# Optimization experiments

Hardware: AMD Instinct MI355X
Metric: run time of the kernel (lower is better)

The kernel has to match this reference:

```python
import jax, jax.numpy as jnp
import numpy as np

B, T, D = 32, 256, 256  # batch, input_length, output_dim (input_dim == output_dim)
SCALE = 0.06  # ~ 1/sqrt(D) glorot-ish init so LSTM gates don't saturate


def hard_sigmoid(x):
    # Keras-1 default inner_activation for LSTM
    return jnp.clip(0.2 * x + 0.5, 0.0, 1.0)


def lstm_cell(x_t, h, c, W, U, b, d):
    # Keras gate order: i, f, c(g), o
    z = x_t @ W + h @ U + b
    i = hard_sigmoid(z[:, :d])
    f = hard_sigmoid(z[:, d:2 * d])
    g = jnp.tanh(z[:, 2 * d:3 * d])
    o = hard_sigmoid(z[:, 3 * d:])
    c_new = f * c + i * g
    h_new = o * jnp.tanh(c_new)
    return h_new, c_new


def setup_inputs() -> dict:
    key = jax.random.key(0)
    ks = jax.random.split(key, 7)
    x = jax.random.normal(ks[0], (B, T, D), dtype=jnp.float32)
    reader_W = jax.random.normal(ks[1], (D, 4 * D), dtype=jnp.float32) * SCALE
    reader_U = jax.random.normal(ks[2], (D, 4 * D), dtype=jnp.float32) * SCALE
    reader_b = jnp.zeros((4 * D,), jnp.float32)
    writer_W = jax.random.normal(ks[3], (2 * D, 4 * D), dtype=jnp.float32) * SCALE
    writer_U = jax.random.normal(ks[4], (D, 4 * D), dtype=jnp.float32) * SCALE
    writer_b = jnp.zeros((4 * D,), jnp.float32)
    composer_W = jax.random.normal(ks[5], (2 * D, 2 * D), dtype=jnp.float32) * SCALE
    composer_b = jnp.zeros((2 * D,), jnp.float32)
    return {"x": x, "reader_W": reader_W, "reader_U": reader_U, "reader_b": reader_b,
            "writer_W": writer_W, "writer_U": writer_U, "writer_b": writer_b,
            "composer_W": composer_W, "composer_b": composer_b}


def reference(x, reader_W, reader_U, reader_b, writer_W, writer_U, writer_b,
              composer_W, composer_b):
    b, t, d = x.shape
    h0 = jnp.zeros((b, d), x.dtype)
    c0 = jnp.zeros((b, d), x.dtype)

    # ---- read: reader LSTM over the sequence (return_sequences) ----
    def rstep(carry, x_t):
        h, c = carry
        h, c = lstm_cell(x_t, h, c, reader_W, reader_U, reader_b, d)
        return (h, c), h

    _, o_seq = jax.lax.scan(rstep, (h0, c0), jnp.swapaxes(x, 0, 1))  # [T,B,D]

    mem0 = x  # mem_0 = input (B, T, D)

    # ---- compose_and_write_step per timestep ----
    def step(carry, o_t):
        mem, wh, wc = carry
        # summarize_memory: eqs 2-3
        scores = jnp.einsum('bd,btd->bt', o_t, mem)
        z_t = jax.nn.softmax(scores, axis=-1)                 # (B, T)
        m_rt = jnp.einsum('bt,btd->bd', z_t, mem)             # (B, D)
        # compose (eq 4), linear activation
        c_t = jnp.concatenate([o_t, m_rt], axis=-1) @ composer_W + composer_b  # (B, 2D)
        # writer LSTM step (eq 5)
        wh, wc = lstm_cell(c_t, wh, wc, writer_W, writer_U, writer_b, d)
        # update_memory (eq 6): blend via tiled z_t / h_t
        zt = z_t[:, :, None]
        mem = mem * (1.0 - zt) + wh[:, None, :] * zt
        return (mem, wh, wc), wh

    (_, _, _), hs = jax.lax.scan(step, (mem0, h0, c0), o_seq)  # hs: [T,B,D]
    return hs[-1]  # return_mode == 'last_output'
```

## Files before the change

### kernel.cpp

```cpp
#include <hip/hip_runtime.h>
#include <math.h>

#define TB 512
#define NBATCH 32
#define TT 256
#define DD 256

typedef float f32x4 __attribute__((ext_vector_type(4)));

#define WS_WF   0u
#define WS_BF   524288u
#define WS_HP   525312u
#define WS_PAR  541696u
#define PS      260
#define WS_WHP  608256u
#define WS_BAR  616448u
#define WS_FLOATS 616832u

#define O_WW    0
#define S_WW    784
#define O_RW    12544
#define S_RW    524
#define O_MEM   20928
#define S_MEM   260
#define O_WACT  29248
#define S_WACT  780
#define O_RACT  35488
#define S_RACT  524
#define O_WZ    39680
#define O_RZ    39840
#define O_SS    40000
#define O_SE    40032
#define O_WC    40064
#define O_RC    40096
#define O_WB    40128
#define O_RB    40144
#define O_RJ    40160
#define O_MS    40224
#define LDS_FLOATS 40352
#define DYN_LDS_BYTES (LDS_FLOATS*4)

__device__ __forceinline__ float hsig(float x) { return fminf(fmaxf(0.2f*x + 0.5f, 0.f), 1.f); }
__device__ __forceinline__ int akw(int k) { return k + 4*(k/192); }
__device__ __forceinline__ int akr(int k) { return k + 4*(k/128); }

__device__ __forceinline__ void gst(float* p, float v) {
  __hip_atomic_store(p, v, __ATOMIC_RELAXED, __HIP_MEMORY_SCOPE_AGENT);
}
__device__ __forceinline__ float gld(const float* p) {
  return __hip_atomic_load(p, __ATOMIC_RELAXED, __HIP_MEMORY_SCOPE_AGENT);
}
__device__ __forceinline__ void gst4(float* p, f32x4 v) {
  asm volatile("global_store_dwordx4 %0, %1, off sc0 sc1" :: "v"(p), "v"(v) : "memory");
}

__device__ __forceinline__ void bar_arrive(int* cnt) {
  asm volatile("s_waitcnt vmcnt(0) lgkmcnt(0)" ::: "memory");
  __syncthreads();
  if (threadIdx.x == 0)
    __hip_atomic_fetch_add(cnt, 1, __ATOMIC_RELAXED, __HIP_MEMORY_SCOPE_AGENT);
}
__device__ __forceinline__ void bar_wait(int* cnt, int target) {
  if (threadIdx.x == 0) {
    int sp = 0;
    while (__hip_atomic_load(cnt, __ATOMIC_RELAXED, __HIP_MEMORY_SCOPE_AGENT) < target) {
      if (++sp > (1 << 20)) break;
    }
  }
  __syncthreads();
}
__device__ __forceinline__ void barrier_fenced(int* cnt, int target) {
  __syncthreads();
  if (threadIdx.x == 0) {
    __threadfence();
    __hip_atomic_fetch_add(cnt, 1, __ATOMIC_RELAXED, __HIP_MEMORY_SCOPE_AGENT);
    int sp = 0;
    while (__hip_atomic_load(cnt, __ATOMIC_RELAXED, __HIP_MEMORY_SCOPE_AGENT) < target) {
      if (++sp > (1 << 20)) break;
    }
    __threadfence();
  }
  __syncthreads();
}

__global__ void __launch_bounds__(TB) nse_kernel(
    const float* __restrict__ x,
    const float* __restrict__ rW, const float* __restrict__ rU, const float* __restrict__ rb,
    const float* __restrict__ wW, const float* __restrict__ wU, const float* __restrict__ wb,
    const float* __restrict__ cW, const float* __restrict__ cb,
    float* __restrict__ out, float* __restrict__ ws)
{
  extern __shared__ float sm[];
  const int tid = threadIdx.x;
  const int w = blockIdx.x;
  const int g = w >> 6;
  const int m = w & 63;
  const int b0 = g * 8;
  const int blm = m >> 3;
  const int isl = m & 7;
  const int bmy = b0 + blm;

  float* Wf   = ws + WS_WF;
  float* bfv  = ws + WS_BF;
  float* hpub = ws + WS_HP;
  float* par  = ws + WS_PAR;
  float* whp  = ws + WS_WHP;
  int*   bars = (int*)(ws + WS_BAR);
  int* gcnt = &bars[8*32];
  int* ccnt = &bars[g*32];

  if (w == 0 && tid == 0) {
    for (int i = 0; i < 9; i++)
      __hip_atomic_store(&bars[i*32], 0, __ATOMIC_RELAXED, __HIP_MEMORY_SCOPE_AGENT);
    __hip_atomic_store(&bars[9*32], 1357911, __ATOMIC_RELEASE, __HIP_MEMORY_SCOPE_AGENT);
  }
  if (tid == 0) {
    int sp = 0;
    while (__hip_atomic_load(&bars[9*32], __ATOMIC_ACQUIRE, __HIP_MEMORY_SCOPE_AGENT) != 1357911) {
      if (++sp > (1 << 20)) break;
    }
  }
  __syncthreads();

  {
    const int kt = w >> 4, nt = w & 15;
    const int r = tid >> 4, c4 = (tid & 15) * 4;
    float a0 = 0.f, a1 = 0.f, a2 = 0.f, a3 = 0.f;
    for (int jc = 0; jc < 512; jc += 32) {
      for (int u = tid; u < 1024; u += TB) {
        int rr = u >> 5, jj = u & 31;
        sm[rr*33 + jj] = cW[(32*kt + rr)*512 + jc + jj];
      }
      {
        int jj = tid >> 4, cc = (tid & 15) * 4;
        const f32x4 v = *(const f32x4*)&wW[(jc + jj)*1024 + 64*nt + cc];
        float* d = &sm[1056 + jj*68 + cc];
        d[0] = v.x; d[1] = v.y; d[2] = v.z; d[3] = v.w;
      }
      __syncthreads();
      #pragma unroll 8
      for (int j = 0; j < 32; j++) {
        const float a = sm[r*33 + j];
        const float* wv = &sm[1056 + j*68 + c4];
        a0 += a*wv[0]; a1 += a*wv[1]; a2 += a*wv[2]; a3 += a*wv[3];
      }
      __syncthreads();
    }
    float* d = &Wf[(32*kt + r)*1024 + 64*nt + c4];
    d[0] = a0; d[1] = a1; d[2] = a2; d[3] = a3;
  }
  if (w >= 16 && w < 32) {
    __syncthreads();
    const int base = (w - 16) * 64;
    const int c = tid & 63, jq = tid >> 6;
    float p = 0.f;
    for (int j = 64*jq; j < 64*jq + 64; j++) p += cb[j] * wW[j*1024 + base + c];
    sm[jq*68 + c] = p;
    __syncthreads();
    if (tid < 64) {
      float s = wb[base + tid];
      for (int j = 0; j < 8; j++) s += sm[j*68 + tid];
      bfv[base + tid] = s;
    }
  }
  barrier_fenced(gcnt, 256);

  for (int u = tid; u < 3072; u += TB) {
    const int k = u >> 2, gate = u & 3;
    const float* sp = (k < 512) ? &Wf[(size_t)k*1024 + gate*256 + 4*m]
                                : &wU[(size_t)(k-512)*1024 + gate*256 + 4*m];
    const f32x4 v = *(const f32x4*)sp;
    const int ik = akw(k);
    sm[O_WW + (gate*4+0)*S_WW + ik] = v.x;
    sm[O_WW + (gate*4+1)*S_WW + ik] = v.y;
    sm[O_WW + (gate*4+2)*S_WW + ik] = v.z;
    sm[O_WW + (gate*4+3)*S_WW + ik] = v.w;
  }
  for (int u = tid; u < 2048; u += TB) {
    const int k = u >> 2, gate = u & 3;
    const float* sp = (k < 256) ? &rW[(size_t)k*1024 + gate*256 + 4*m]
                                : &rU[(size_t)(k-256)*1024 + gate*256 + 4*m];
    const f32x4 v = *(const f32x4*)sp;
    const int ik = akr(k);
    sm[O_RW + (gate*4+0)*S_RW + ik] = v.x;
    sm[O_RW + (gate*4+1)*S_RW + ik] = v.y;
    sm[O_RW + (gate*4+2)*S_RW + ik] = v.z;
    sm[O_RW + (gate*4+3)*S_RW + ik] = v.w;
  }
  for (int u = tid; u < 2048; u += TB) {
    const int r = u >> 6, d4 = (u & 63) * 4;
    *(f32x4*)&sm[O_MEM + r*S_MEM + d4] =
        *(const f32x4*)&x[((size_t)bmy*TT + 32*isl + r)*DD + d4];
  }
  for (int u = tid; u < LDS_FLOATS - O_WACT; u += TB) sm[O_WACT + u] = 0.f;
  if (tid < 16) {
    const int gate = tid >> 2, dl = tid & 3;
    sm[O_WB + tid] = bfv[gate*256 + 4*m + dl];
    sm[O_RB + tid] = rb[gate*256 + 4*m + dl];
  }
  __syncthreads();

  int bphase = 0;
  for (int s = 0; s <= TT; s++) {
    {
      const int bl = tid >> 6, d4 = (tid & 63) * 4;
      f32x4 vh, vw;
      const float* ph = &hpub[(size_t)((s+1)&1)*8192 + (b0+bl)*256 + d4];
      const float* pw = &whp[(b0+bl)*256 + d4];
      asm volatile(
        "global_load_dwordx4 %0, %2, off sc0 sc1\n\t"
        "global_load_dwordx4 %1, %3, off sc0 sc1\n\t"
        "s_waitcnt vmcnt(0)"
        : "=&v"(vh), "=&v"(vw) : "v"(ph), "v"(pw) : "memory");
      if (s >= 1) {
        *(f32x4*)&sm[O_RACT + bl*S_RACT + akr(256 + d4)] = vh;
        *(f32x4*)&sm[O_WACT + bl*S_WACT + akw(d4)]       = vh;
      }
      if (s >= 2)
        *(f32x4*)&sm[O_WACT + bl*S_WACT + akw(512 + d4)] = vw;
      if (s <= TT-1)
        *(f32x4*)&sm[O_RACT + bl*S_RACT + akr(d4)] =
            *(const f32x4*)&x[((size_t)(b0+bl)*TT + s)*DD + d4];
    }
    __syncthreads();

    if (s >= 1) {
      const int r = tid >> 4, tk = tid & 15;
      float* mrow = &sm[O_MEM + r*S_MEM + 16*tk];
      const float* orow = &sm[O_RACT + blm*S_RACT + akr(256 + 16*tk)];
      float acc = 0.f;
      if (s >= 2) {
        const float zr = sm[O_SE + r] * sm[O_RJ + blm*8 + isl];
        const float omz = 1.f - zr;
        const float* hrow = &sm[O_WACT + blm*S_WACT + akw(512 + 16*tk)];
        #pragma unroll
        for (int i2 = 0; i2 < 16; i2 += 4) {
          f32x4 mv = *(f32x4*)(mrow + i2);
          const f32x4 hv = *(const f32x4*)(hrow + i2);
          const f32x4 ov = *(const f32x4*)(orow + i2);
          mv.x = mv.x*omz + hv.x*zr;  mv.y = mv.y*omz + hv.y*zr;
          mv.z = mv.z*omz + hv.z*zr;  mv.w = mv.w*omz + hv.w*zr;
          *(f32x4*)(mrow + i2) = mv;
          acc += mv.x*ov.x + mv.y*ov.y + mv.z*ov.z + mv.w*ov.w;
        }
      } else {
        #pragma unroll
        for (int i2 = 0; i2 < 16; i2 += 4) {
          const f32x4 mv = *(const f32x4*)(mrow + i2);
          const f32x4 ov = *(const f32x4*)(orow + i2);
          acc += mv.x*ov.x + mv.y*ov.y + mv.z*ov.z + mv.w*ov.w;
        }
      }
      acc += __shfl_xor(acc, 1, 64); acc += __shfl_xor(acc, 2, 64);
      acc += __shfl_xor(acc, 4, 64); acc += __shfl_xor(acc, 8, 64);
      if (tk == 0) sm[O_SS + r] = acc;
    }
    __syncthreads();
    if (s >= 1 && tid < 32) {
      const float sc = sm[O_SS + tid];
      float mx = sc;
      mx = fmaxf(mx, __shfl_xor(mx, 1, 64)); mx = fmaxf(mx, __shfl_xor(mx, 2, 64));
      mx = fmaxf(mx, __shfl_xor(mx, 4, 64)); mx = fmaxf(mx, __shfl_xor(mx, 8, 64));
      mx = fmaxf(mx, __shfl_xor(mx, 16, 64));
      const float e = __expf(sc - mx);
      float su = e;
      su += __shfl_xor(su, 1, 64); su += __shfl_xor(su, 2, 64); su += __shfl_xor(su, 4, 64);
      su += __shfl_xor(su, 8, 64); su += __shfl_xor(su, 16, 64);
      sm[O_SE + tid] = e;
      if (tid == 0) {
        gst(&par[((size_t)bmy*8 + isl)*PS + 256], mx);
        gst(&par[((size_t)bmy*8 + isl)*PS + 257], su);
      }
    }
    __syncthreads();
    if (s >= 1) {
      const int dblk = tid >> 3, rh = tid & 7;
      f32x4 p; p.x = 0.f; p.y = 0.f; p.z = 0.f; p.w = 0.f;
      #pragma unroll
      for (int i = 0; i < 4; i++) {
        const int rr = 4*rh + i;
        const float e = sm[O_SE + rr];
        const f32x4 mv = *(const f32x4*)&sm[O_MEM + rr*S_MEM + 4*dblk];
        p.x += e*mv.x; p.y += e*mv.y; p.z += e*mv.z; p.w += e*mv.w;
      }
      p.x += __shfl_xor(p.x,1,64); p.x += __shfl_xor(p.x,2,64); p.x += __shfl_xor(p.x,4,64);
      p.y += __shfl_xor(p.y,1,64); p.y += __shfl_xor(p.y,2,64); p.y += __shfl_xor(p.y,4,64);
      p.z += __shfl_xor(p.z,1,64); p.z += __shfl_xor(p.z,2,64); p.z += __shfl_xor(p.z,4,64);
      p.w += __shfl_xor(p.w,1,64); p.w += __shfl_xor(p.w,2,64); p.w += __shfl_xor(p.w,4,64);
      if (rh == 0) gst4(&par[((size_t)bmy*8 + isl)*PS + 4*dblk], p);
    }
    ++bphase; bar_arrive(ccnt);

    if (s <= TT-1) {
      const int q  = tid & 3;
      const int cl = ((tid >> 4) & 3) + 4 * (tid >> 7);
      const int bl = ((tid >> 2) & 3) + 4 * ((tid >> 6) & 1);
      const float* wr = &sm[O_RW + cl*S_RW + 132*q];
      const float* ar = &sm[O_RACT + bl*S_RACT + 132*q];
      float acc = 0.f;
      #pragma unroll
      for (int kk = 0; kk < 128; kk += 4) {
        const f32x4 wv = *(const f32x4*)(wr + kk);
        const f32x4 av = *(const f32x4*)(ar + kk);
        acc += wv.x*av.x + wv.y*av.y + wv.z*av.z + wv.w*av.w;
      }
      acc += __shfl_xor(acc, 1, 64);
      acc += __shfl_xor(acc, 2, 64);
      if (q == 0) sm[O_RZ + bl*20 + cl] = acc + sm[O_RB + cl];
    }
    __syncthreads();
    if (s <= TT-1 && tid < 32) {
      const int bl = tid >> 2, dl = tid & 3;
      const float zi = sm[O_RZ + bl*20 + dl];
      const float zf = sm[O_RZ + bl*20 + 4 + dl];
      const float zg = sm[O_RZ + bl*20 + 8 + dl];
      const float zo = sm[O_RZ + bl*20 + 12 + dl];
      const float cn = hsig(zf)*sm[O_RC + tid] + hsig(zi)*tanhf(zg);
      sm[O_RC + tid] = cn;
      gst(&hpub[(size_t)(s&1)*8192 + (b0+bl)*256 + 4*m + dl], hsig(zo)*tanhf(cn));
    }
    bar_wait(ccnt, 64*bphase);

    if (s >= 1) {
      if (tid < 128) {
        const int bl = tid >> 4, j = (tid >> 1) & 7, h2 = tid & 1;
        sm[O_MS + bl*16 + j*2 + h2] = gld(&par[((size_t)(b0+bl)*8 + j)*PS + 256 + h2]);
      }
      __syncthreads();
      if (tid < 8) {
        const int bl = tid;
        float M = sm[O_MS + bl*16];
        for (int j = 1; j < 8; j++) M = fmaxf(M, sm[O_MS + bl*16 + 2*j]);
        float tot = 0.f, f0[8];
        for (int j = 0; j < 8; j++) {
          f0[j] = __expf(sm[O_MS + bl*16 + 2*j] - M);
          tot += f0[j] * sm[O_MS + bl*16 + 2*j + 1];
        }
        const float inv = 1.f / tot;
        for (int j = 0; j < 8; j++) sm[O_RJ + bl*8 + j] = f0[j]*inv;
      }
      __syncthreads();
      {
        const int bl = tid >> 6, d4 = (tid & 63) * 4;
        const float* p0 = &par[((size_t)(b0+bl)*8 + 0)*PS + d4];
        const float* p4 = p0 + 4*PS;
        f32x4 v0,v1,v2,v3,v4,v5,v6,v7;
        asm volatile(
          "global_load_dwordx4 %0, %8, off sc0 sc1\n\t"
          "global_load_dwordx4 %1, %8, off offset:1040 sc0 sc1\n\t"
          "global_load_dwordx4 %2, %8, off offset:2080 sc0 sc1\n\t"
          "global_load_dwordx4 %3, %8, off offset:3120 sc0 sc1\n\t"
          "global_load_dwordx4 %4, %9, off sc0 sc1\n\t"
          "global_load_dwordx4 %5, %9, off offset:1040 sc0 sc1\n\t"
          "global_load_dwordx4 %6, %9, off offset:2080 sc0 sc1\n\t"
          "global_load_dwordx4 %7, %9, off offset:3120 sc0 sc1\n\t"
          "s_waitcnt vmcnt(0)"
          : "=&v"(v0),"=&v"(v1),"=&v"(v2),"=&v"(v3),
            "=&v"(v4),"=&v"(v5),"=&v"(v6),"=&v"(v7)
          : "v"(p0), "v"(p4) : "memory");
        const float* rj = &sm[O_RJ + bl*8];
        f32x4 a;
        a.x = rj[0]*v0.x + rj[1]*v1.x + rj[2]*v2.x + rj[3]*v3.x
            + rj[4]*v4.x + rj[5]*v5.x + rj[6]*v6.x + rj[7]*v7.x;
        a.y = rj[0]*v0.y + rj[1]*v1.y + rj[2]*v2.y + rj[3]*v3.y
            + rj[4]*v4.y + rj[5]*v5.y + rj[6]*v6.y + rj[7]*v7.y;
        a.z = rj[0]*v0.z + rj[1]*v1.z + rj[2]*v2.z + rj[3]*v3.z
            + rj[4]*v4.z + rj[5]*v5.z + rj[6]*v6.z + rj[7]*v7.z;
        a.w = rj[0]*v0.w + rj[1]*v1.w + rj[2]*v2.w + rj[3]*v3.w
            + rj[4]*v4.w + rj[5]*v5.w + rj[6]*v6.w + rj[7]*v7.w;
        *(f32x4*)&sm[O_WACT + bl*S_WACT + akw(256 + d4)] = a;
      }
      __syncthreads();
      {
        const int q  = tid & 3;
        const int cl = ((tid >> 4) & 3) + 4 * (tid >> 7);
        const int bl = ((tid >> 2) & 3) + 4 * ((tid >> 6) & 1);
        const float* wr = &sm[O_WW + cl*S_WW + 196*q];
        const float* ar = &sm[O_WACT + bl*S_WACT + 196*q];
        float acc = 0.f;
        #pragma unroll
        for (int kk = 0; kk < 192; kk += 4) {
          const f32x4 wv = *(const f32x4*)(wr + kk);
          const f32x4 av = *(const f32x4*)(ar + kk);
          acc += wv.x*av.x + wv.y*av.y + wv.z*av.z + wv.w*av.w;
        }
        acc += __shfl_xor(acc, 1, 64);
        acc += __shfl_xor(acc, 2, 64);
        if (q == 0) sm[O_WZ + bl*20 + cl] = acc + sm[O_WB + cl];
      }
      __syncthreads();
      if (tid < 32) {
        const int bl = tid >> 2, dl = tid & 3;
        const float zi = sm[O_WZ + bl*20 + dl];
        const float zf = sm[O_WZ + bl*20 + 4 + dl];
        const float zg = sm[O_WZ + bl*20 + 8 + dl];
        const float zo = sm[O_WZ + bl*20 + 12 + dl];
        const float cn = hsig(zf)*sm[O_WC + tid] + hsig(zi)*tanhf(zg);
        sm[O_WC + tid] = cn;
        const float hn = hsig(zo)*tanhf(cn);
        if (s == TT) out[(b0+bl)*256 + 4*m + dl] = hn;
        else         gst(&whp[(b0+bl)*256 + 4*m + dl], hn);
      }
    }
    ++bphase; bar_arrive(ccnt);
    bar_wait(ccnt, 64*bphase);
  }
}

extern "C" void kernel_launch(void* const* d_in, const int* in_sizes, int n_in,
                              void* d_out, int out_size, void* d_ws, size_t ws_size,
                              hipStream_t stream) {
  (void)in_sizes; (void)n_in;
  if (ws_size < (size_t)WS_FLOATS * 4u) {
    hipMemsetAsync(d_out, 0, (size_t)out_size * 4u, stream);
    return;
  }
  const float* x  = (const float*)d_in[0];
  const float* rW = (const float*)d_in[1];
  const float* rU = (const float*)d_in[2];
  const float* rb = (const float*)d_in[3];
  const float* wW = (const float*)d_in[4];
  const float* wU = (const float*)d_in[5];
  const float* wb = (const float*)d_in[6];
  const float* cW = (const float*)d_in[7];
  const float* cb = (const float*)d_in[8];
  float* out = (float*)d_out;
  float* ws  = (float*)d_ws;

  hipFuncSetAttribute((const void*)nse_kernel,
                      hipFuncAttributeMaxDynamicSharedMemorySize, DYN_LDS_BYTES);

  void* args[] = { (void*)&x, (void*)&rW, (void*)&rU, (void*)&rb,
                   (void*)&wW, (void*)&wU, (void*)&wb, (void*)&cW, (void*)&cb,
                   (void*)&out, (void*)&ws };
  hipError_t err = hipLaunchCooperativeKernel((const void*)nse_kernel,
                                              dim3(256), dim3(TB), args,
                                              DYN_LDS_BYTES, stream);
  if (err != hipSuccess) {
    nse_kernel<<<dim3(256), dim3(TB), DYN_LDS_BYTES, stream>>>(
        x, rW, rU, rb, wW, wU, wb, cW, cb, out, ws);
  }
}
```

Measured before the change: 3.129 ms.

## Replace counter barriers with per-block flags and overlap independent work across barriers

Replaces the atomic-counter group barrier with per-block phase flags that one wavefront polls with a wave-wide vote. It also moves the writer matvec terms that do not depend on the composed memory vector (h and wh parts) ahead of the barrier wait. The softmax-stat load is merged with the partial-sum loads into a single batch, and the next x row is prefetched between arrive and wait. The shared-memory layout is unified to one padding scheme. The aim is to shorten the serial critical path per timestep. The cost is more flag memory and a reduced spin timeout.

```diff
diff --git a/kernel.cpp b/kernel.cpp
--- a/kernel.cpp
+++ b/kernel.cpp
@@ -15,34 +15,33 @@
 #define PS      260
 #define WS_WHP  608256u
 #define WS_BAR  616448u
-#define WS_FLOATS 616832u
+#define WS_FLOATS 624704u
 
 #define O_WW    0
-#define S_WW    784
-#define O_RW    12544
+#define S_WW    792
+#define O_RW    12672
 #define S_RW    524
-#define O_MEM   20928
+#define O_MEM   21056
 #define S_MEM   260
-#define O_WACT  29248
-#define S_WACT  780
-#define O_RACT  35488
+#define O_WACT  29376
+#define S_WACT  792
+#define O_RACT  35712
 #define S_RACT  524
-#define O_WZ    39680
-#define O_RZ    39840
-#define O_SS    40000
-#define O_SE    40032
-#define O_WC    40064
-#define O_RC    40096
-#define O_WB    40128
-#define O_RB    40144
-#define O_RJ    40160
-#define O_MS    40224
-#define LDS_FLOATS 40352
+#define O_WZ    39904
+#define O_RZ    40064
+#define O_SS    40224
+#define O_SE    40256
+#define O_WC    40288
+#define O_RC    40320
+#define O_WB    40352
+#define O_RB    40368
+#define O_RJ    40384
+#define O_MS    40448
+#define LDS_FLOATS 40576
 #define DYN_LDS_BYTES (LDS_FLOATS*4)
 
 __device__ __forceinline__ float hsig(float x) { return fminf(fmaxf(0.2f*x + 0.5f, 0.f), 1.f); }
-__device__ __forceinline__ int akw(int k) { return k + 4*(k/192); }
-__device__ __forceinline__ int akr(int k) { return k + 4*(k/128); }
+__device__ __forceinline__ int ak(int k) { return k + 4*(k/128); }
 
 __device__ __forceinline__ void gst(float* p, float v) {
   __hip_atomic_store(p, v, __ATOMIC_RELAXED, __HIP_MEMORY_SCOPE_AGENT);
@@ -54,17 +53,20 @@
   asm volatile("global_store_dwordx4 %0, %1, off sc0 sc1" :: "v"(p), "v"(v) : "memory");
 }
 
-__device__ __forceinline__ void bar_arrive(int* cnt) {
+__device__ __forceinline__ void bar_arrive(int* myflag, int phase) {
   asm volatile("s_waitcnt vmcnt(0) lgkmcnt(0)" ::: "memory");
   __syncthreads();
   if (threadIdx.x == 0)
-    __hip_atomic_fetch_add(cnt, 1, __ATOMIC_RELAXED, __HIP_MEMORY_SCOPE_AGENT);
-}
-__device__ __forceinline__ void bar_wait(int* cnt, int target) {
-  if (threadIdx.x == 0) {
+    __hip_atomic_store(myflag, phase, __ATOMIC_RELAXED, __HIP_MEMORY_SCOPE_AGENT);
+}
+__device__ __forceinline__ void bar_wait(int* flags, int phase) {
+  if (threadIdx.x < 64) {
     int sp = 0;
-    while (__hip_atomic_load(cnt, __ATOMIC_RELAXED, __HIP_MEMORY_SCOPE_AGENT) < target) {
-      if (++sp > (1 << 20)) break;
+    for (;;) {
+      const int v = __hip_atomic_load(&flags[threadIdx.x*32], __ATOMIC_RELAXED,
+                                      __HIP_MEMORY_SCOPE_AGENT);
+      if (__all(v >= phase)) break;
+      if (++sp > (1 << 16)) break;
     }
   }
   __syncthreads();
@@ -106,17 +108,18 @@
   float* par  = ws + WS_PAR;
   float* whp  = ws + WS_WHP;
   int*   bars = (int*)(ws + WS_BAR);
-  int* gcnt = &bars[8*32];
-  int* ccnt = &bars[g*32];
+  int* flg    = &bars[g*2048];
+  int* myflag = &bars[g*2048 + m*32];
+  int* lcnt   = &bars[8192];
+  int* magic  = &bars[8192 + 32];
 
   if (w == 0 && tid == 0) {
-    for (int i = 0; i < 9; i++)
-      __hip_atomic_store(&bars[i*32], 0, __ATOMIC_RELAXED, __HIP_MEMORY_SCOPE_AGENT);
-    __hip_atomic_store(&bars[9*32], 1357911, __ATOMIC_RELEASE, __HIP_MEMORY_SCOPE_AGENT);
+    __hip_atomic_store(lcnt, 0, __ATOMIC_RELAXED, __HIP_MEMORY_SCOPE_AGENT);
+    __hip_atomic_store(magic, 1357911, __ATOMIC_RELEASE, __HIP_MEMORY_SCOPE_AGENT);
   }
   if (tid == 0) {
     int sp = 0;
-    while (__hip_atomic_load(&bars[9*32], __ATOMIC_ACQUIRE, __HIP_MEMORY_SCOPE_AGENT) != 1357911) {
+    while (__hip_atomic_load(magic, __ATOMIC_ACQUIRE, __HIP_MEMORY_SCOPE_AGENT) != 1357911) {
       if (++sp > (1 << 20)) break;
     }
   }
@@ -163,14 +166,14 @@
       bfv[base + tid] = s;
     }
   }
-  barrier_fenced(gcnt, 256);
+  barrier_fenced(lcnt, 256);
 
   for (int u = tid; u < 3072; u += TB) {
     const int k = u >> 2, gate = u & 3;
     const float* sp = (k < 512) ? &Wf[(size_t)k*1024 + gate*256 + 4*m]
                                 : &wU[(size_t)(k-512)*1024 + gate*256 + 4*m];
     const f32x4 v = *(const f32x4*)sp;
-    const int ik = akw(k);
+    const int ik = ak(k);
     sm[O_WW + (gate*4+0)*S_WW + ik] = v.x;
     sm[O_WW + (gate*4+1)*S_WW + ik] = v.y;
     sm[O_WW + (gate*4+2)*S_WW + ik] = v.z;
@@ -181,7 +184,7 @@
     const float* sp = (k < 256) ? &rW[(size_t)k*1024 + gate*256 + 4*m]
                                 : &rU[(size_t)(k-256)*1024 + gate*256 + 4*m];
     const f32x4 v = *(const f32x4*)sp;
-    const int ik = akr(k);
+    const int ik = ak(k);
     sm[O_RW + (gate*4+0)*S_RW + ik] = v.x;
     sm[O_RW + (gate*4+1)*S_RW + ik] = v.y;
     sm[O_RW + (gate*4+2)*S_RW + ik] = v.z;
@@ -193,12 +196,22 @@
         *(const f32x4*)&x[((size_t)bmy*TT + 32*isl + r)*DD + d4];
   }
   for (int u = tid; u < LDS_FLOATS - O_WACT; u += TB) sm[O_WACT + u] = 0.f;
+  {
+    const int bl = tid >> 6, d4 = (tid & 63) * 4;
+    *(f32x4*)&sm[O_RACT + bl*S_RACT + ak(d4)] =
+        *(const f32x4*)&x[(size_t)(b0+bl)*TT*DD + d4];
+  }
   if (tid < 16) {
     const int gate = tid >> 2, dl = tid & 3;
     sm[O_WB + tid] = bfv[gate*256 + 4*m + dl];
     sm[O_RB + tid] = rb[gate*256 + 4*m + dl];
   }
   __syncthreads();
+
+  const int q  = tid & 3;
+  const int cl = ((tid >> 4) & 3) + 4 * (tid >> 7);
+  const int bl8 = ((tid >> 2) & 3) + 4 * ((tid >> 6) & 1);
+  const int qo = (q >> 1) * 132 + (q & 1) * 64;
 
   int bphase = 0;
   for (int s = 0; s <= TT; s++) {
@@ -213,26 +226,23 @@
         "s_waitcnt vmcnt(0)"
         : "=&v"(vh), "=&v"(vw) : "v"(ph), "v"(pw) : "memory");
       if (s >= 1) {
-        *(f32x4*)&sm[O_RACT + bl*S_RACT + akr(256 + d4)] = vh;
-        *(f32x4*)&sm[O_WACT + bl*S_WACT + akw(d4)]       = vh;
+        *(f32x4*)&sm[O_RACT + bl*S_RACT + ak(256 + d4)] = vh;
+        *(f32x4*)&sm[O_WACT + bl*S_WACT + ak(d4)]       = vh;
       }
       if (s >= 2)
-        *(f32x4*)&sm[O_WACT + bl*S_WACT + akw(512 + d4)] = vw;
-      if (s <= TT-1)
-        *(f32x4*)&sm[O_RACT + bl*S_RACT + akr(d4)] =
-            *(const f32x4*)&x[((size_t)(b0+bl)*TT + s)*DD + d4];
+        *(f32x4*)&sm[O_WACT + bl*S_WACT + ak(512 + d4)] = vw;
     }
     __syncthreads();
 
     if (s >= 1) {
       const int r = tid >> 4, tk = tid & 15;
       float* mrow = &sm[O_MEM + r*S_MEM + 16*tk];
-      const float* orow = &sm[O_RACT + blm*S_RACT + akr(256 + 16*tk)];
+      const float* orow = &sm[O_RACT + blm*S_RACT + ak(256 + 16*tk)];
       float acc = 0.f;
       if (s >= 2) {
         const float zr = sm[O_SE + r] * sm[O_RJ + blm*8 + isl];
         const float omz = 1.f - zr;
-        const float* hrow = &sm[O_WACT + blm*S_WACT + akw(512 + 16*tk)];
+        const float* hrow = &sm[O_WACT + blm*S_WACT + ak(512 + 16*tk)];
         #pragma unroll
         for (int i2 = 0; i2 < 16; i2 += 4) {
           f32x4 mv = *(f32x4*)(mrow + i2);
@@ -289,14 +299,12 @@
       p.w += __shfl_xor(p.w,1,64); p.w += __shfl_xor(p.w,2,64); p.w += __shfl_xor(p.w,4,64);
       if (rh == 0) gst4(&par[((size_t)bmy*8 + isl)*PS + 4*dblk], p);
     }
-    ++bphase; bar_arrive(ccnt);
-
+    ++bphase; bar_arrive(myflag, bphase);
+
+    float accw = 0.f;
     if (s <= TT-1) {
-      const int q  = tid & 3;
-      const int cl = ((tid >> 4) & 3) + 4 * (tid >> 7);
-      const int bl = ((tid >> 2) & 3) + 4 * ((tid >> 6) & 1);
       const float* wr = &sm[O_RW + cl*S_RW + 132*q];
-      const float* ar = &sm[O_RACT + bl*S_RACT + 132*q];
+      const float* ar = &sm[O_RACT + bl8*S_RACT + 132*q];
       float acc = 0.f;
       #pragma unroll
       for (int kk = 0; kk < 128; kk += 4) {
@@ -306,7 +314,20 @@
       }
       acc += __shfl_xor(acc, 1, 64);
       acc += __shfl_xor(acc, 2, 64);
-      if (q == 0) sm[O_RZ + bl*20 + cl] = acc + sm[O_RB + cl];
+      if (q == 0) sm[O_RZ + bl8*20 + cl] = acc + sm[O_RB + cl];
+    }
+    if (s >= 1) {
+      const float* wr = &sm[O_WW + cl*S_WW];
+      const float* ar = &sm[O_WACT + bl8*S_WACT];
+      #pragma unroll
+      for (int kk = 0; kk < 64; kk += 4) {
+        const f32x4 w0 = *(const f32x4*)(wr + qo + kk);
+        const f32x4 a0 = *(const f32x4*)(ar + qo + kk);
+        const f32x4 w2 = *(const f32x4*)(wr + 528 + qo + kk);
+        const f32x4 a2 = *(const f32x4*)(ar + 528 + qo + kk);
+        accw += w0.x*a0.x + w0.y*a0.y + w0.z*a0.z + w0.w*a0.w;
+        accw += w2.x*a2.x + w2.y*a2.y + w2.z*a2.z + w2.w*a2.w;
+      }
     }
     __syncthreads();
     if (s <= TT-1 && tid < 32) {
@@ -319,45 +340,48 @@
       sm[O_RC + tid] = cn;
       gst(&hpub[(size_t)(s&1)*8192 + (b0+bl)*256 + 4*m + dl], hsig(zo)*tanhf(cn));
     }
-    bar_wait(ccnt, 64*bphase);
+    bar_wait(flg, bphase);
 
     if (s >= 1) {
-      if (tid < 128) {
-        const int bl = tid >> 4, j = (tid >> 1) & 7, h2 = tid & 1;
-        sm[O_MS + bl*16 + j*2 + h2] = gld(&par[((size_t)(b0+bl)*8 + j)*PS + 256 + h2]);
-      }
+      const int bl = tid >> 6, d4 = (tid & 63) * 4;
+      f32x4 v0,v1,v2,v3,v4,v5,v6,v7;
+      float msv;
+      {
+        const float* p0 = &par[((size_t)(b0+bl)*8 + 0)*PS + d4];
+        const float* p4 = p0 + 4*PS;
+        const int idx = tid & 127;
+        const float* msp = &par[((size_t)(b0 + (idx>>4))*8 + ((idx>>1)&7))*PS + 256 + (idx&1)];
+        asm volatile(
+          "global_load_dwordx4 %0, %9, off sc0 sc1\n\t"
+          "global_load_dwordx4 %1, %9, off offset:1040 sc0 sc1\n\t"
+          "global_load_dwordx4 %2, %9, off offset:2080 sc0 sc1\n\t"
+          "global_load_dwordx4 %3, %9, off offset:3120 sc0 sc1\n\t"
+          "global_load_dwordx4 %4, %10, off sc0 sc1\n\t"
+          "global_load_dwordx4 %5, %10, off offset:1040 sc0 sc1\n\t"
+          "global_load_dwordx4 %6, %10, off offset:2080 sc0 sc1\n\t"
+          "global_load_dwordx4 %7, %10, off offset:3120 sc0 sc1\n\t"
+          "global_load_dword   %8, %11, off sc0 sc1\n\t"
+          "s_waitcnt vmcnt(0)"
+          : "=&v"(v0),"=&v"(v1),"=&v"(v2),"=&v"(v3),
+            "=&v"(v4),"=&v"(v5),"=&v"(v6),"=&v"(v7),"=&v"(msv)
+          : "v"(p0), "v"(p4), "v"(msp) : "memory");
+      }
+      if (tid < 128) sm[O_MS + tid] = msv;
       __syncthreads();
       if (tid < 8) {
-        const int bl = tid;
-        float M = sm[O_MS + bl*16];
-        for (int j = 1; j < 8; j++) M = fmaxf(M, sm[O_MS + bl*16 + 2*j]);
+        const int bl2 = tid;
+        float M = sm[O_MS + bl2*16];
+        for (int j = 1; j < 8; j++) M = fmaxf(M, sm[O_MS + bl2*16 + 2*j]);
         float tot = 0.f, f0[8];
         for (int j = 0; j < 8; j++) {
-          f0[j] = __expf(sm[O_MS + bl*16 + 2*j] - M);
-          tot += f0[j] * sm[O_MS + bl*16 + 2*j + 1];
+          f0[j] = __expf(sm[O_MS + bl2*16 + 2*j] - M);
+          tot += f0[j] * sm[O_MS + bl2*16 + 2*j + 1];
         }
         const float inv = 1.f / tot;
-        for (int j = 0; j < 8; j++) sm[O_RJ + bl*8 + j] = f0[j]*inv;
+        for (int j = 0; j < 8; j++) sm[O_RJ + bl2*8 + j] = f0[j]*inv;
       }
       __syncthreads();
       {
-        const int bl = tid >> 6, d4 = (tid & 63) * 4;
-        const float* p0 = &par[((size_t)(b0+bl)*8 + 0)*PS + d4];
-        const float* p4 = p0 + 4*PS;
-        f32x4 v0,v1,v2,v3,v4,v5,v6,v7;
-        asm volatile(
-          "global_load_dwordx4 %0, %8, off sc0 sc1\n\t"
-          "global_load_dwordx4 %1, %8, off offset:1040 sc0 sc1\n\t"
-          "global_load_dwordx4 %2, %8, off offset:2080 sc0 sc1\n\t"
-          "global_load_dwordx4 %3, %8, off offset:3120 sc0 sc1\n\t"
-          "global_load_dwordx4 %4, %9, off sc0 sc1\n\t"
-          "global_load_dwordx4 %5, %9, off offset:1040 sc0 sc1\n\t"
-          "global_load_dwordx4 %6, %9, off offset:2080 sc0 sc1\n\t"
-          "global_load_dwordx4 %7, %9, off offset:3120 sc0 sc1\n\t"
-          "s_waitcnt vmcnt(0)"
-          : "=&v"(v0),"=&v"(v1),"=&v"(v2),"=&v"(v3),
-            "=&v"(v4),"=&v"(v5),"=&v"(v6),"=&v"(v7)
-          : "v"(p0), "v"(p4) : "memory");
         const float* rj = &sm[O_RJ + bl*8];
         f32x4 a;
         a.x = rj[0]*v0.x + rj[1]*v1.x + rj[2]*v2.x + rj[3]*v3.x
@@ -368,42 +392,44 @@
             + rj[4]*v4.z + rj[5]*v5.z + rj[6]*v6.z + rj[7]*v7.z;
         a.w = rj[0]*v0.w + rj[1]*v1.w + rj[2]*v2.w + rj[3]*v3.w
             + rj[4]*v4.w + rj[5]*v5.w + rj[6]*v6.w + rj[7]*v7.w;
-        *(f32x4*)&sm[O_WACT + bl*S_WACT + akw(256 + d4)] = a;
+        *(f32x4*)&sm[O_WACT + bl*S_WACT + ak(256 + d4)] = a;
       }
       __syncthreads();
       {
-        const int q  = tid & 3;
-        const int cl = ((tid >> 4) & 3) + 4 * (tid >> 7);
-        const int bl = ((tid >> 2) & 3) + 4 * ((tid >> 6) & 1);
-        const float* wr = &sm[O_WW + cl*S_WW + 196*q];
-        const float* ar = &sm[O_WACT + bl*S_WACT + 196*q];
-        float acc = 0.f;
+        const float* wr = &sm[O_WW + cl*S_WW + 264 + qo];
+        const float* ar = &sm[O_WACT + bl8*S_WACT + 264 + qo];
         #pragma unroll
-        for (int kk = 0; kk < 192; kk += 4) {
+        for (int kk = 0; kk < 64; kk += 4) {
           const f32x4 wv = *(const f32x4*)(wr + kk);
           const f32x4 av = *(const f32x4*)(ar + kk);
-          acc += wv.x*av.x + wv.y*av.y + wv.z*av.z + wv.w*av.w;
+          accw += wv.x*av.x + wv.y*av.y + wv.z*av.z + wv.w*av.w;
         }
-        acc += __shfl_xor(acc, 1, 64);
-        acc += __shfl_xor(acc, 2, 64);
-        if (q == 0) sm[O_WZ + bl*20 + cl] = acc + sm[O_WB + cl];
+        accw += __shfl_xor(accw, 1, 64);
+        accw += __shfl_xor(accw, 2, 64);
+        if (q == 0) sm[O_WZ + bl8*20 + cl] = accw + sm[O_WB + cl];
       }
       __syncthreads();
       if (tid < 32) {
-        const int bl = tid >> 2, dl = tid & 3;
-        const float zi = sm[O_WZ + bl*20 + dl];
-        const float zf = sm[O_WZ + bl*20 + 4 + dl];
-        const float zg = sm[O_WZ + bl*20 + 8 + dl];
-        const float zo = sm[O_WZ + bl*20 + 12 + dl];
+        const int bl2 = tid >> 2, dl = tid & 3;
+        const float zi = sm[O_WZ + bl2*20 + dl];
+        const float zf = sm[O_WZ + bl2*20 + 4 + dl];
+        const float zg = sm[O_WZ + bl2*20 + 8 + dl];
+        const float zo = sm[O_WZ + bl2*20 + 12 + dl];
         const float cn = hsig(zf)*sm[O_WC + tid] + hsig(zi)*tanhf(zg);
         sm[O_WC + tid] = cn;
         const float hn = hsig(zo)*tanhf(cn);
-        if (s == TT) out[(b0+bl)*256 + 4*m + dl] = hn;
-        else         gst(&whp[(b0+bl)*256 + 4*m + dl], hn);
-      }
-    }
-    ++bphase; bar_arrive(ccnt);
-    bar_wait(ccnt, 64*bphase);
+        if (s == TT) out[(b0+bl2)*256 + 4*m + dl] = hn;
+        else         gst(&whp[(b0+bl2)*256 + 4*m + dl], hn);
+      }
+    }
+    if (s == TT) break;
+    ++bphase; bar_arrive(myflag, bphase);
+    if (s <= TT-2) {
+      const int bl = tid >> 6, d4 = (tid & 63) * 4;
+      *(f32x4*)&sm[O_RACT + bl*S_RACT + ak(d4)] =
+          *(const f32x4*)&x[((size_t)(b0+bl)*TT + s + 1)*DD + d4];
+    }
+    bar_wait(flg, bphase);
   }
 }
 
```

Measured after the change: 3.154 ms. No clear change (+0.8%).
